# Kernel optimization log

Hardware: AMD Instinct MI355X
Metric: run time of the kernel (lower is better)

The kernel has to match this reference:

```python
import jax, jax.numpy as jnp
import numpy as np
import math

N = 100000
E = 3200000
NFEAT = 128
NHID = 256
NCLASS = 16


def _uniform(key, shape, stdv):
    return jax.random.uniform(key, shape, jnp.float32, -stdv, stdv)


def setup_inputs() -> dict:
    key = jax.random.key(0)
    ks = jax.random.split(key, 16)
    x = jax.random.normal(ks[0], (N, NFEAT), jnp.float32)
    adj_row = jax.random.randint(ks[1], (E,), 0, N, jnp.int32)
    adj_col = jax.random.randint(ks[2], (E,), 0, N, jnp.int32)
    adj_val = jax.random.uniform(ks[3], (E,), jnp.float32)

    def gc_params(kw, kb, fin, fout):
        stdv = 1.0 / math.sqrt(fout)
        return _uniform(kw, (fin, fout), stdv), _uniform(kb, (fout,), stdv)

    w1, b1 = gc_params(ks[4], ks[5], NFEAT, NHID)
    w2, b2 = gc_params(ks[6], ks[7], NHID, NHID)
    w3, b3 = gc_params(ks[8], ks[9], NHID, NHID)
    w4, b4 = gc_params(ks[10], ks[11], NHID, NHID)
    fc_stdv = 1.0 / math.sqrt(NHID)
    fc_w = _uniform(ks[12], (NHID, NCLASS), fc_stdv)
    fc_b = _uniform(ks[13], (NCLASS,), fc_stdv)
    return {
        "x": x, "adj_val": adj_val,
        "w1": w1, "b1": b1, "w2": w2, "b2": b2,
        "w3": w3, "b3": b3, "w4": w4, "b4": b4,
        "fc_w": fc_w, "fc_b": fc_b,
        "adj_row": adj_row, "adj_col": adj_col,
    }


def _spmm(row, col, val, dense):
    # (sparse [N,N]) @ dense[N,D]: gather source rows, weight, scatter-add to dest
    msgs = dense[col] * val[:, None]  # [E, D]
    return jax.ops.segment_sum(msgs, row, num_segments=N)


def _gc_layer(x, row, col, val, w, b):
    support = x @ w              # dense GEMM [N, fout]
    out = _spmm(row, col, val, support)
    return out + b


def reference(x, adj_val, w1, b1, w2, b2, w3, b3, w4, b4, fc_w, fc_b, adj_row, adj_col):
    h = jax.nn.relu(_gc_layer(x, adj_row, adj_col, adj_val, w1, b1))
    h = jax.nn.relu(_gc_layer(h, adj_row, adj_col, adj_val, w2, b2))
    h = jax.nn.relu(_gc_layer(h, adj_row, adj_col, adj_val, w3, b3))
    h = jax.nn.relu(_gc_layer(h, adj_row, adj_col, adj_val, w4, b4))
    logits = h @ fc_w + fc_b
    return jax.nn.log_softmax(logits, axis=1)
```

## Files before the change

kernel.cpp:

```cpp
#include <hip/hip_runtime.h>
#include <hip/hip_bf16.h>

#define NN 100000
#define EE 3200000
#define NF 128
#define NH 256
#define NC 16
#define NB ((NN + 255) >> 8)
#define TILEA 8192
#define NBLKA ((EE + TILEA - 1) / TILEA)

typedef __bf16 bf16x8 __attribute__((ext_vector_type(8)));
typedef float f32x4 __attribute__((ext_vector_type(4)));
typedef float f32x2 __attribute__((ext_vector_type(2)));

static __device__ __forceinline__ unsigned short f2bf(float f) {
    unsigned int u = __builtin_bit_cast(unsigned int, f);
    u += 0x7FFFu + ((u >> 16) & 1u);
    return (unsigned short)(u >> 16);
}
static __device__ __forceinline__ float b2f(unsigned short h) {
    unsigned int u = ((unsigned int)h) << 16;
    return __builtin_bit_cast(float, u);
}
static __device__ __forceinline__ unsigned char f2fp8(float v) {
    return (unsigned char)(__builtin_amdgcn_cvt_pk_fp8_f32(v, v, 0, false) & 0xFF);
}

__global__ void k_cvt_fp8(const float* __restrict__ in, unsigned char* __restrict__ out, int n) {
    int i = (blockIdx.x * blockDim.x + threadIdx.x) * 4;
    if (i + 3 < n) {
        float4 v = *(const float4*)(in + i);
        int r = __builtin_amdgcn_cvt_pk_fp8_f32(v.x, v.y, 0, false);
        r = __builtin_amdgcn_cvt_pk_fp8_f32(v.z, v.w, r, true);
        *(unsigned int*)(out + i) = (unsigned int)r;
    } else {
        for (int t = 0; t < 4 && i + t < n; ++t) out[i + t] = f2fp8(in[i + t]);
    }
}

__global__ void k_wT(const float* __restrict__ W, unsigned short* __restrict__ Wt, int K, int C) {
    int i = blockIdx.x * blockDim.x + threadIdx.x;
    if (i < K * C) {
        int k = i / C, c = i % C;
        Wt[c * K + k] = f2bf(W[i]);
    }
}

__global__ __launch_bounds__(256) void k_cnt(const int* __restrict__ row, int* __restrict__ cmat, int e) {
    __shared__ int hist[NB];
    int tid = threadIdx.x;
    int tile0 = blockIdx.x * TILEA;
    for (int b = tid; b < NB; b += 256) hist[b] = 0;
    __syncthreads();
#pragma unroll 8
    for (int t = 0; t < TILEA / 256; ++t) {
        int i = tile0 + t * 256 + tid;
        if (i < e) atomicAdd(&hist[row[i] >> 8], 1);
    }
    __syncthreads();
    for (int b = tid; b < NB; b += 256) cmat[b * NBLKA + blockIdx.x] = hist[b];
}

__global__ __launch_bounds__(512) void k_csum(int* __restrict__ cmat, int* __restrict__ btot) {
    __shared__ int lds[512];
    int b = blockIdx.x, tid = threadIdx.x;
    int v = (tid < NBLKA) ? cmat[b * NBLKA + tid] : 0;
    lds[tid] = v; __syncthreads();
    for (int off = 1; off < 512; off <<= 1) {
        int add = (tid >= off) ? lds[tid - off] : 0;
        __syncthreads();
        lds[tid] += add;
        __syncthreads();
    }
    if (tid < NBLKA) cmat[b * NBLKA + tid] = lds[tid] - v;
    if (tid == 511) btot[b] = lds[511];
}

__global__ __launch_bounds__(512) void k_bscan(const int* __restrict__ btot, int* __restrict__ bbase) {
    __shared__ int lds[512];
    int tid = threadIdx.x;
    int v = (tid < NB) ? btot[tid] : 0;
    lds[tid] = v; __syncthreads();
    for (int off = 1; off < 512; off <<= 1) {
        int add = (tid >= off) ? lds[tid - off] : 0;
        __syncthreads();
        lds[tid] += add;
        __syncthreads();
    }
    if (tid < NB) bbase[tid] = lds[tid] - v;
    if (tid == NB - 1) bbase[NB] = lds[tid];
}

__global__ __launch_bounds__(256) void k_scat2(const int* __restrict__ row, const int* __restrict__ col,
                                               const float* __restrict__ val, const int* __restrict__ cmat,
                                               const int* __restrict__ bbase,
                                               unsigned long long* __restrict__ tmp, int e) {
    __shared__ int hist[NB];
    __shared__ int base[NB];
    int tid = threadIdx.x;
    int tile0 = blockIdx.x * TILEA;
    for (int b = tid; b < NB; b += 256) {
        base[b] = bbase[b] + cmat[b * NBLKA + blockIdx.x];
        hist[b] = 0;
    }
    __syncthreads();
#pragma unroll 8
    for (int t = 0; t < TILEA / 256; ++t) {
        int i = tile0 + t * 256 + tid;
        if (i < e) {
            int r = row[i];
            int b = r >> 8;
            int rk = atomicAdd(&hist[b], 1);
            unsigned long long rec = ((unsigned long long)__builtin_bit_cast(unsigned int, val[i]) << 32)
                                   | (unsigned int)(col[i] | ((r & 255) << 17));
            tmp[base[b] + rk] = rec;
        }
    }
}

__global__ __launch_bounds__(256) void k_binB2(const int* __restrict__ bbase,
                                               const unsigned long long* __restrict__ tmp,
                                               unsigned long long* __restrict__ pairs,
                                               int* __restrict__ rowp, int n) {
    __shared__ int hist[256];
    __shared__ int cur[256];
    int tid = threadIdx.x;
    int b = blockIdx.x;
    int r0 = b << 8;
    int s = bbase[b], e = bbase[b + 1];
    hist[tid] = 0;
    __syncthreads();
    for (int i = s + tid; i < e; i += 256) {
        int r = ((unsigned int)tmp[i] >> 17) & 255;
        atomicAdd(&hist[r], 1);
    }
    __syncthreads();
    int v = hist[tid];
    for (int off = 1; off < 256; off <<= 1) {
        int add = (tid >= off) ? hist[tid - off] : 0;
        __syncthreads();
        hist[tid] += add;
        __syncthreads();
    }
    int pos0 = s + hist[tid] - v;
    int rr = r0 + tid;
    if (rr < n) rowp[rr] = pos0;
    if (b == 0 && tid == 0) rowp[n] = bbase[NB];
    cur[tid] = pos0;
    __syncthreads();
    for (int i = s + tid; i < e; i += 256) {
        unsigned long long rec = tmp[i];
        unsigned int w = (unsigned int)rec;
        int r = (w >> 17) & 255;
        int pos = atomicAdd(&cur[r], 1);
        pairs[pos] = (rec & 0xFFFFFFFF00000000ULL) | (unsigned long long)(w & 0x1FFFFu);
    }
}

template <bool BR, bool F8>
__global__ __launch_bounds__(256) void k_gemm(const unsigned short* __restrict__ A,
                                              const unsigned short* __restrict__ Bt,
                                              const float* __restrict__ bias,
                                              unsigned short* __restrict__ C,
                                              unsigned char* __restrict__ C8,
                                              int M, int K) {
    int wave = threadIdx.x >> 6, lane = threadIdx.x & 63;
    int row0 = blockIdx.x * 64;
    int colBase = wave * 64;
    int hr = lane & 15, kg = lane >> 4;
    f32x4 acc[4][4];
#pragma unroll
    for (int r = 0; r < 4; ++r)
#pragma unroll
        for (int c = 0; c < 4; ++c) acc[r][c] = (f32x4){0.f, 0.f, 0.f, 0.f};

    for (int k0 = 0; k0 < K; k0 += 32) {
        int kk = k0 + kg * 8;
        bf16x8 af[4], bf_[4];
#pragma unroll
        for (int r = 0; r < 4; ++r) {
            int ar = row0 + r * 16 + hr;
            if (ar >= M) ar = M - 1;
            af[r] = *(const bf16x8*)(A + (size_t)ar * K + kk);
        }
#pragma unroll
        for (int c = 0; c < 4; ++c) {
            int bc = colBase + c * 16 + hr;
            bf_[c] = *(const bf16x8*)(Bt + (size_t)bc * K + kk);
        }
#pragma unroll
        for (int r = 0; r < 4; ++r)
#pragma unroll
            for (int c = 0; c < 4; ++c)
                acc[r][c] = __builtin_amdgcn_mfma_f32_16x16x32_bf16(af[r], bf_[c], acc[r][c], 0, 0, 0);
    }
#pragma unroll
    for (int r = 0; r < 4; ++r)
#pragma unroll
        for (int c = 0; c < 4; ++c) {
            int col = colBase + c * 16 + hr;
            float bv = BR ? bias[col] : 0.f;
#pragma unroll
            for (int i = 0; i < 4; ++i) {
                int rr = row0 + r * 16 + kg * 4 + i;
                float v = acc[r][c][i];
                if (BR) v = fmaxf(v + bv, 0.f);
                if (rr < M) {
                    if (F8) C8[(size_t)rr * 256 + col] = f2fp8(v);
                    else    C[(size_t)rr * 256 + col] = f2bf(v);
                }
            }
        }
}

__global__ __launch_bounds__(256) void k_spmm256(const int* __restrict__ rowp,
                                                 const unsigned long long* __restrict__ pairs,
                                                 const unsigned char* __restrict__ S,
                                                 const float* __restrict__ bias,
                                                 unsigned short* __restrict__ Hout, int n) {
    int lane = threadIdx.x & 63;
    int row = blockIdx.x * 4 + (threadIdx.x >> 6);
    if (row >= n) return;
    int s = rowp[row], e = rowp[row + 1];
    int f = lane * 4;
    float a0 = 0.f, a1 = 0.f, a2 = 0.f, a3 = 0.f;
#pragma unroll 8
    for (int i = s; i < e; ++i) {
        unsigned long long p = pairs[i];
        unsigned int c = (unsigned int)p;
        float v = __builtin_bit_cast(float, (unsigned int)(p >> 32));
        int w = *(const int*)(S + (size_t)c * 256 + f);
        f32x2 dlo = __builtin_amdgcn_cvt_pk_f32_fp8(w, false);
        f32x2 dhi = __builtin_amdgcn_cvt_pk_f32_fp8(w, true);
        a0 += v * dlo.x; a1 += v * dlo.y; a2 += v * dhi.x; a3 += v * dhi.y;
    }
    float4 bv = *(const float4*)(bias + f);
    a0 = fmaxf(a0 + bv.x, 0.f);
    a1 = fmaxf(a1 + bv.y, 0.f);
    a2 = fmaxf(a2 + bv.z, 0.f);
    a3 = fmaxf(a3 + bv.w, 0.f);
    ushort4 o; o.x = f2bf(a0); o.y = f2bf(a1); o.z = f2bf(a2); o.w = f2bf(a3);
    *(ushort4*)(Hout + (size_t)row * 256 + f) = o;
}

__global__ __launch_bounds__(256) void k_spmm128(const int* __restrict__ rowp,
                                                 const unsigned long long* __restrict__ pairs,
                                                 const unsigned char* __restrict__ X,
                                                 unsigned short* __restrict__ Out, int n) {
    int lane = threadIdx.x & 63;
    int row = blockIdx.x * 4 + (threadIdx.x >> 6);
    if (row >= n) return;
    int s = rowp[row], e = rowp[row + 1];
    int f = lane * 2;
    float a0 = 0.f, a1 = 0.f;
#pragma unroll 8
    for (int i = s; i < e; ++i) {
        unsigned long long p = pairs[i];
        unsigned int c = (unsigned int)p;
        float v = __builtin_bit_cast(float, (unsigned int)(p >> 32));
        int w = (int)*(const unsigned short*)(X + (size_t)c * 128 + f);
        f32x2 d = __builtin_amdgcn_cvt_pk_f32_fp8(w, false);
        a0 += v * d.x; a1 += v * d.y;
    }
    ushort2 o; o.x = f2bf(a0); o.y = f2bf(a1);
    *(ushort2*)(Out + (size_t)row * 128 + f) = o;
}

__global__ __launch_bounds__(256) void k_fc_lsm(const unsigned short* __restrict__ H,
                                                const float* __restrict__ Wf,
                                                const float* __restrict__ bf,
                                                float* __restrict__ out, int n) {
    int lane = threadIdx.x & 63;
    int wave = threadIdx.x >> 6;
    int sub = lane >> 4, j = lane & 15;
    int node = (blockIdx.x * 4 + wave) * 4 + sub;
    bool valid = node < n;
    int nd = valid ? node : (n - 1);
    float acc = 0.f;
    for (int f0 = 0; f0 < NH; f0 += 8) {
        union { uint4 u; unsigned short s[8]; } h;
        h.u = *(const uint4*)(H + (size_t)nd * NH + f0);
#pragma unroll
        for (int t = 0; t < 8; ++t) acc += b2f(h.s[t]) * Wf[(f0 + t) * NC + j];
    }
    acc += bf[j];
    float mx = acc;
    for (int m = 1; m < 16; m <<= 1) mx = fmaxf(mx, __shfl_xor(mx, m, 16));
    float sm = __expf(acc - mx);
    for (int m = 1; m < 16; m <<= 1) sm += __shfl_xor(sm, m, 16);
    float res = acc - mx - __logf(sm);
    if (valid) out[(size_t)node * NC + j] = res;
}

extern "C" void kernel_launch(void* const* d_in, const int* in_sizes, int n_in,
                              void* d_out, int out_size, void* d_ws, size_t ws_size,
                              hipStream_t stream) {
    const float* x      = (const float*)d_in[0];
    const float* adjval = (const float*)d_in[1];
    const float* w1 = (const float*)d_in[2];  const float* b1 = (const float*)d_in[3];
    const float* w2 = (const float*)d_in[4];  const float* b2 = (const float*)d_in[5];
    const float* w3 = (const float*)d_in[6];  const float* b3 = (const float*)d_in[7];
    const float* w4 = (const float*)d_in[8];  const float* b4 = (const float*)d_in[9];
    const float* fcw = (const float*)d_in[10]; const float* fcb = (const float*)d_in[11];
    const int* arow = (const int*)d_in[12];
    const int* acol = (const int*)d_in[13];
    float* out = (float*)d_out;

    char* ws = (char*)d_ws;
    size_t off = 0;
    auto alloc = [&](size_t bytes) { size_t o = off; off += (bytes + 255) & ~(size_t)255; return o; };

    unsigned char*  xb  = (unsigned char*)(ws + alloc((size_t)NN * NF));
    unsigned short* Sb  = (unsigned short*)(ws + alloc((size_t)NN * NH * 2));
    unsigned short* H1  = (unsigned short*)(ws + alloc((size_t)NN * NH * 2));
    unsigned short* H2  = (unsigned short*)(ws + alloc((size_t)NN * NH * 2));
    unsigned short* Wt1 = (unsigned short*)(ws + alloc((size_t)NH * NF * 2));
    unsigned short* Wt2 = (unsigned short*)(ws + alloc((size_t)NH * NH * 2));
    unsigned short* Wt3 = (unsigned short*)(ws + alloc((size_t)NH * NH * 2));
    unsigned short* Wt4 = (unsigned short*)(ws + alloc((size_t)NH * NH * 2));
    int*   rowp   = (int*)(ws + alloc(((size_t)NN + 1) * 4));
    int*   cmat   = (int*)(ws + alloc((size_t)NB * NBLKA * 4));
    int*   btot   = (int*)(ws + alloc((size_t)NB * 4));
    int*   bbase  = (int*)(ws + alloc(((size_t)NB + 1) * 4));
    unsigned long long* pairs = (unsigned long long*)(ws + alloc((size_t)EE * 8));
    unsigned long long* tmp = (unsigned long long*)H2;
    unsigned char* S8 = (unsigned char*)Sb;

    k_cvt_fp8<<<(NN * NF / 4 + 255) / 256, 256, 0, stream>>>(x, xb, NN * NF);
    k_wT<<<(NF * NH + 255) / 256, 256, 0, stream>>>(w1, Wt1, NF, NH);
    k_wT<<<(NH * NH + 255) / 256, 256, 0, stream>>>(w2, Wt2, NH, NH);
    k_wT<<<(NH * NH + 255) / 256, 256, 0, stream>>>(w3, Wt3, NH, NH);
    k_wT<<<(NH * NH + 255) / 256, 256, 0, stream>>>(w4, Wt4, NH, NH);

    k_cnt<<<NBLKA, 256, 0, stream>>>(arow, cmat, EE);
    k_csum<<<NB, 512, 0, stream>>>(cmat, btot);
    k_bscan<<<1, 512, 0, stream>>>(btot, bbase);
    k_scat2<<<NBLKA, 256, 0, stream>>>(arow, acol, adjval, cmat, bbase, tmp, EE);
    k_binB2<<<NB, 256, 0, stream>>>(bbase, tmp, pairs, rowp, NN);

    int gGemm = (NN + 63) / 64;
    int gSpmm = (NN + 3) / 4;
    k_spmm128<<<gSpmm, 256, 0, stream>>>(rowp, pairs, xb, Sb, NN);
    k_gemm<true, false><<<gGemm, 256, 0, stream>>>(Sb, Wt1, b1, H1, nullptr, NN, NF);
    k_gemm<false, true><<<gGemm, 256, 0, stream>>>(H1, Wt2, nullptr, nullptr, S8, NN, NH);
    k_spmm256<<<gSpmm, 256, 0, stream>>>(rowp, pairs, S8, b2, H2, NN);
    k_gemm<false, true><<<gGemm, 256, 0, stream>>>(H2, Wt3, nullptr, nullptr, S8, NN, NH);
    k_spmm256<<<gSpmm, 256, 0, stream>>>(rowp, pairs, S8, b3, H1, NN);
    k_gemm<false, true><<<gGemm, 256, 0, stream>>>(H1, Wt4, nullptr, nullptr, S8, NN, NH);
    k_spmm256<<<gSpmm, 256, 0, stream>>>(rowp, pairs, S8, b4, H2, NN);
    k_fc_lsm<<<(NN + 15) / 16, 256, 0, stream>>>(H2, fcw, fcb, out, NN);
}
```

Baseline: 995.6 us.

## Pack edge records to 32 bits, stage GEMM A tiles in LDS, fuse weight transposes

Each CSR edge record shrinks from 64 to 32 bits: the column index keeps 17 bits and the edge weight is stored as a 15-bit truncated bf16-like value in the high bits. This halves pair traffic in every SpMM pass at the cost of weight precision. The GEMM now double-buffers A tiles into LDS using global_load_lds, with a barrier each k step. The four weight-transpose launches are merged into one, and the SpMM accumulators use packed f32x2 math.

```diff
diff --git a/kernel.cpp b/kernel.cpp
--- a/kernel.cpp
+++ b/kernel.cpp
@@ -26,6 +26,10 @@
 static __device__ __forceinline__ unsigned char f2fp8(float v) {
     return (unsigned char)(__builtin_amdgcn_cvt_pk_fp8_f32(v, v, 0, false) & 0xFF);
 }
+
+#define GLOAD_LDS16(g, l) __builtin_amdgcn_global_load_lds( \
+    (const __attribute__((address_space(1))) unsigned int*)(g), \
+    (__attribute__((address_space(3))) unsigned int*)(l), 16, 0, 0)
 
 __global__ void k_cvt_fp8(const float* __restrict__ in, unsigned char* __restrict__ out, int n) {
     int i = (blockIdx.x * blockDim.x + threadIdx.x) * 4;
@@ -39,12 +43,23 @@
     }
 }
 
-__global__ void k_wT(const float* __restrict__ W, unsigned short* __restrict__ Wt, int K, int C) {
+__global__ void k_wT4(const float* __restrict__ w1, const float* __restrict__ w2,
+                      const float* __restrict__ w3, const float* __restrict__ w4,
+                      unsigned short* __restrict__ Wt1, unsigned short* __restrict__ Wt2,
+                      unsigned short* __restrict__ Wt3, unsigned short* __restrict__ Wt4) {
     int i = blockIdx.x * blockDim.x + threadIdx.x;
-    if (i < K * C) {
-        int k = i / C, c = i % C;
-        Wt[c * K + k] = f2bf(W[i]);
-    }
+    if (i < NF * NH) {
+        int k = i / NH, c = i % NH;
+        Wt1[c * NF + k] = f2bf(w1[i]);
+        return;
+    }
+    i -= NF * NH;
+    int seg = i >> 16;
+    int j = i & 65535;
+    const float* W = (seg == 0) ? w2 : (seg == 1) ? w3 : w4;
+    unsigned short* Wt = (seg == 0) ? Wt2 : (seg == 1) ? Wt3 : Wt4;
+    int k = j >> 8, c = j & 255;
+    Wt[c * NH + k] = f2bf(W[j]);
 }
 
 __global__ __launch_bounds__(256) void k_cnt(const int* __restrict__ row, int* __restrict__ cmat, int e) {
@@ -121,7 +136,7 @@
 
 __global__ __launch_bounds__(256) void k_binB2(const int* __restrict__ bbase,
                                                const unsigned long long* __restrict__ tmp,
-                                               unsigned long long* __restrict__ pairs,
+                                               unsigned int* __restrict__ pairs,
                                                int* __restrict__ rowp, int n) {
     __shared__ int hist[256];
     __shared__ int cur[256];
@@ -153,8 +168,11 @@
         unsigned long long rec = tmp[i];
         unsigned int w = (unsigned int)rec;
         int r = (w >> 17) & 255;
+        unsigned int vb = (unsigned int)(rec >> 32);
+        unsigned int bf = (vb + 0x7FFFu + ((vb >> 16) & 1u)) >> 16;
+        unsigned int v15 = (bf + 1u) >> 1;
         int pos = atomicAdd(&cur[r], 1);
-        pairs[pos] = (rec & 0xFFFFFFFF00000000ULL) | (unsigned long long)(w & 0x1FFFFu);
+        pairs[pos] = (v15 << 17) | (w & 0x1FFFFu);
     }
 }
 
@@ -165,25 +183,36 @@
                                               unsigned short* __restrict__ C,
                                               unsigned char* __restrict__ C8,
                                               int M, int K) {
-    int wave = threadIdx.x >> 6, lane = threadIdx.x & 63;
+    __shared__ unsigned short Atile[2][64 * 32];
+    int tid = threadIdx.x;
+    int wave = tid >> 6, lane = tid & 63;
     int row0 = blockIdx.x * 64;
     int colBase = wave * 64;
     int hr = lane & 15, kg = lane >> 4;
+
+    int srow = tid >> 2;
+    int selem = (tid & 3) * 8;
+    int arow = row0 + srow; if (arow >= M) arow = M - 1;
+    const unsigned short* srcBase = A + (size_t)arow * K + selem;
+
     f32x4 acc[4][4];
 #pragma unroll
     for (int r = 0; r < 4; ++r)
 #pragma unroll
         for (int c = 0; c < 4; ++c) acc[r][c] = (f32x4){0.f, 0.f, 0.f, 0.f};
 
+    GLOAD_LDS16(srcBase, &Atile[0][0] + (size_t)tid * 8);
+    __syncthreads();
+
+    int cur = 0;
     for (int k0 = 0; k0 < K; k0 += 32) {
+        if (k0 + 32 < K)
+            GLOAD_LDS16(srcBase + k0 + 32, &Atile[cur ^ 1][0] + (size_t)tid * 8);
+        bf16x8 af[4], bf_[4];
         int kk = k0 + kg * 8;
-        bf16x8 af[4], bf_[4];
-#pragma unroll
-        for (int r = 0; r < 4; ++r) {
-            int ar = row0 + r * 16 + hr;
-            if (ar >= M) ar = M - 1;
-            af[r] = *(const bf16x8*)(A + (size_t)ar * K + kk);
-        }
+#pragma unroll
+        for (int r = 0; r < 4; ++r)
+            af[r] = *(const bf16x8*)(&Atile[cur][(r * 16 + hr) * 32 + kg * 8]);
 #pragma unroll
         for (int c = 0; c < 4; ++c) {
             int bc = colBase + c * 16 + hr;
@@ -194,6 +223,8 @@
 #pragma unroll
             for (int c = 0; c < 4; ++c)
                 acc[r][c] = __builtin_amdgcn_mfma_f32_16x16x32_bf16(af[r], bf_[c], acc[r][c], 0, 0, 0);
+        __syncthreads();
+        cur ^= 1;
     }
 #pragma unroll
     for (int r = 0; r < 4; ++r)
@@ -215,7 +246,7 @@
 }
 
 __global__ __launch_bounds__(256) void k_spmm256(const int* __restrict__ rowp,
-                                                 const unsigned long long* __restrict__ pairs,
+                                                 const unsigned int* __restrict__ pairs,
                                                  const unsigned char* __restrict__ S,
                                                  const float* __restrict__ bias,
                                                  unsigned short* __restrict__ Hout, int n) {
@@ -224,28 +255,28 @@
     if (row >= n) return;
     int s = rowp[row], e = rowp[row + 1];
     int f = lane * 4;
-    float a0 = 0.f, a1 = 0.f, a2 = 0.f, a3 = 0.f;
+    f32x2 a01 = {0.f, 0.f}, a23 = {0.f, 0.f};
 #pragma unroll 8
     for (int i = s; i < e; ++i) {
-        unsigned long long p = pairs[i];
-        unsigned int c = (unsigned int)p;
-        float v = __builtin_bit_cast(float, (unsigned int)(p >> 32));
+        unsigned int p = pairs[i];
+        unsigned int c = p & 0x1FFFFu;
+        float v = __builtin_bit_cast(float, p & 0xFFFE0000u);
         int w = *(const int*)(S + (size_t)c * 256 + f);
         f32x2 dlo = __builtin_amdgcn_cvt_pk_f32_fp8(w, false);
         f32x2 dhi = __builtin_amdgcn_cvt_pk_f32_fp8(w, true);
-        a0 += v * dlo.x; a1 += v * dlo.y; a2 += v * dhi.x; a3 += v * dhi.y;
+        a01 += dlo * v; a23 += dhi * v;
     }
     float4 bv = *(const float4*)(bias + f);
-    a0 = fmaxf(a0 + bv.x, 0.f);
-    a1 = fmaxf(a1 + bv.y, 0.f);
-    a2 = fmaxf(a2 + bv.z, 0.f);
-    a3 = fmaxf(a3 + bv.w, 0.f);
+    float a0 = fmaxf(a01.x + bv.x, 0.f);
+    float a1 = fmaxf(a01.y + bv.y, 0.f);
+    float a2 = fmaxf(a23.x + bv.z, 0.f);
+    float a3 = fmaxf(a23.y + bv.w, 0.f);
     ushort4 o; o.x = f2bf(a0); o.y = f2bf(a1); o.z = f2bf(a2); o.w = f2bf(a3);
     *(ushort4*)(Hout + (size_t)row * 256 + f) = o;
 }
 
 __global__ __launch_bounds__(256) void k_spmm128(const int* __restrict__ rowp,
-                                                 const unsigned long long* __restrict__ pairs,
+                                                 const unsigned int* __restrict__ pairs,
                                                  const unsigned char* __restrict__ X,
                                                  unsigned short* __restrict__ Out, int n) {
     int lane = threadIdx.x & 63;
@@ -253,17 +284,17 @@
     if (row >= n) return;
     int s = rowp[row], e = rowp[row + 1];
     int f = lane * 2;
-    float a0 = 0.f, a1 = 0.f;
+    f32x2 a01 = {0.f, 0.f};
 #pragma unroll 8
     for (int i = s; i < e; ++i) {
-        unsigned long long p = pairs[i];
-        unsigned int c = (unsigned int)p;
-        float v = __builtin_bit_cast(float, (unsigned int)(p >> 32));
+        unsigned int p = pairs[i];
+        unsigned int c = p & 0x1FFFFu;
+        float v = __builtin_bit_cast(float, p & 0xFFFE0000u);
         int w = (int)*(const unsigned short*)(X + (size_t)c * 128 + f);
         f32x2 d = __builtin_amdgcn_cvt_pk_f32_fp8(w, false);
-        a0 += v * d.x; a1 += v * d.y;
-    }
-    ushort2 o; o.x = f2bf(a0); o.y = f2bf(a1);
+        a01 += d * v;
+    }
+    ushort2 o; o.x = f2bf(a01.x); o.y = f2bf(a01.y);
     *(ushort2*)(Out + (size_t)row * 128 + f) = o;
 }
 
@@ -323,15 +354,12 @@
     int*   cmat   = (int*)(ws + alloc((size_t)NB * NBLKA * 4));
     int*   btot   = (int*)(ws + alloc((size_t)NB * 4));
     int*   bbase  = (int*)(ws + alloc(((size_t)NB + 1) * 4));
-    unsigned long long* pairs = (unsigned long long*)(ws + alloc((size_t)EE * 8));
+    unsigned int* pairs = (unsigned int*)(ws + alloc((size_t)EE * 4));
     unsigned long long* tmp = (unsigned long long*)H2;
     unsigned char* S8 = (unsigned char*)Sb;
 
     k_cvt_fp8<<<(NN * NF / 4 + 255) / 256, 256, 0, stream>>>(x, xb, NN * NF);
-    k_wT<<<(NF * NH + 255) / 256, 256, 0, stream>>>(w1, Wt1, NF, NH);
-    k_wT<<<(NH * NH + 255) / 256, 256, 0, stream>>>(w2, Wt2, NH, NH);
-    k_wT<<<(NH * NH + 255) / 256, 256, 0, stream>>>(w3, Wt3, NH, NH);
-    k_wT<<<(NH * NH + 255) / 256, 256, 0, stream>>>(w4, Wt4, NH, NH);
+    k_wT4<<<(NF * NH + 3 * NH * NH) / 256, 256, 0, stream>>>(w1, w2, w3, w4, Wt1, Wt2, Wt3, Wt4);
 
     k_cnt<<<NBLKA, 256, 0, stream>>>(arow, cmat, EE);
     k_csum<<<NB, 512, 0, stream>>>(cmat, btot);
```

New measurement: 903.6 us. -9.2%, faster.
